# Performance work log

Measured on AMD Instinct MI355X. Metric: run time of the kernel, lower is better.

## Reference

```python
import jax, jax.numpy as jnp
import numpy as np

B = 4096          # graph pairs in batch
NPG = 40          # nodes per molecular graph
N = B * NPG       # total nodes per drug batch
EPG = 160         # directed edges per graph
E = B * EPG
F_IN = 78         # atom feature dim
HID = 128
HEADS = 4
ADD = 8           # additional features (concentrations)
BN_EPS = 1e-5
D0 = HEADS * HID          # 512
CMB = 4 * HID + ADD       # 2 drugs * (mean||max of 128) + ADD = 520


def setup_inputs() -> dict:
    key = jax.random.key(0)
    ks = iter(jax.random.split(key, 64))
    def nrm(shape, s=0.1):
        return jax.random.normal(next(ks), shape, jnp.float32) * s
    def pos(shape):  # positive running variances
        return jax.random.uniform(next(ks), shape, jnp.float32, 0.5, 1.5)
    offs = jnp.repeat(jnp.arange(B, dtype=jnp.int32) * NPG, EPG)
    def edges():
        return jax.random.randint(next(ks), (2, E), 0, NPG, dtype=jnp.int32) + offs[None, :]
    batch = jnp.repeat(jnp.arange(B, dtype=jnp.int32), NPG)
    inp = dict(
        x_a=nrm((N, F_IN), 1.0), edge_a=edges(), batch_a=batch,
        x_b=nrm((N, F_IN), 1.0), edge_b=edges(), batch_b=batch,
        addf=nrm((B, ADD), 1.0),
        # shared GAT encoder params
        gW0=nrm((F_IN, D0)), gb0=nrm((D0,)), gas0=nrm((D0,)), gad0=nrm((D0,)),
        gW1=nrm((D0, D0)), gb1=nrm((D0,)), gas1=nrm((D0,)), gad1=nrm((D0,)),
        gW2=nrm((D0, HID)), gb2=nrm((HID,)), gas2=nrm((HID,)), gad2=nrm((HID,)),
        bn0g=pos((D0,)), bn0b=nrm((D0,)), bn0m=nrm((D0,)), bn0v=pos((D0,)),
        bn1g=pos((D0,)), bn1b=nrm((D0,)), bn1m=nrm((D0,)), bn1v=pos((D0,)),
        bn2g=pos((HID,)), bn2b=nrm((HID,)), bn2m=nrm((HID,)), bn2v=pos((HID,)),
        # combination MLP params (Linear + eval BatchNorm stats)
        mW0=nrm((CMB, 2 * HID)), mb0=nrm((2 * HID,)),
        mg0=pos((2 * HID,)), mbe0=nrm((2 * HID,)), mm0=nrm((2 * HID,)), mv0=pos((2 * HID,)),
        mW1=nrm((2 * HID, HID)), mb1=nrm((HID,)),
        mg1=pos((HID,)), mbe1=nrm((HID,)), mm1=nrm((HID,)), mv1=pos((HID,)),
        mW2=nrm((HID, 1)), mb2=nrm((1,)),
    )
    return inp


def _bn(x, g, b, m, v):
    return (x - m) * jax.lax.rsqrt(v + BN_EPS) * g + b


def _gat(x, src, dst, W, b, a_src, a_dst, heads, ch, concat):
    """PyG GATConv (eval): linear, per-head additive attention with
    leaky_relu(0.2), segment-softmax over incoming edges (self-loops included)."""
    n = x.shape[0]
    h = (x @ W).reshape(n, heads, ch)                     # [N, H, C]
    es = jnp.sum(h * a_src.reshape(1, heads, ch), -1)     # [N, H]
    ed = jnp.sum(h * a_dst.reshape(1, heads, ch), -1)     # [N, H]
    e = jax.nn.leaky_relu(es[src] + ed[dst], 0.2)         # [E', H]
    emax = jax.ops.segment_max(e, dst, num_segments=n)
    ex = jnp.exp(e - emax[dst])
    den = jax.ops.segment_sum(ex, dst, num_segments=n)
    alpha = ex / den[dst]                                 # [E', H]
    out = jax.ops.segment_sum(h[src] * alpha[..., None], dst, num_segments=n)
    out = out.reshape(n, heads * ch) if concat else jnp.mean(out, axis=1)
    return out + b


def _encode(x, edge, batch, p):
    n = x.shape[0]
    sl = jnp.arange(n, dtype=edge.dtype)                  # self-loops (PyG default)
    src = jnp.concatenate([edge[0], sl])
    dst = jnp.concatenate([edge[1], sl])
    x = _gat(x, src, dst, p['gW0'], p['gb0'], p['gas0'], p['gad0'], HEADS, HID, True)
    x = jax.nn.relu(_bn(x, p['bn0g'], p['bn0b'], p['bn0m'], p['bn0v']))
    x = _gat(x, src, dst, p['gW1'], p['gb1'], p['gas1'], p['gad1'], HEADS, HID, True)
    x = jax.nn.relu(_bn(x, p['bn1g'], p['bn1b'], p['bn1m'], p['bn1v']))
    x = _gat(x, src, dst, p['gW2'], p['gb2'], p['gas2'], p['gad2'], 1, HID, False)
    x = _bn(x, p['bn2g'], p['bn2b'], p['bn2m'], p['bn2v'])  # no relu on last layer
    cnt = jax.ops.segment_sum(jnp.ones((n, 1), x.dtype), batch, num_segments=B)
    x_mean = jax.ops.segment_sum(x, batch, num_segments=B) / cnt
    x_max = jax.ops.segment_max(x, batch, num_segments=B)
    return jnp.concatenate([x_mean, x_max], axis=1)        # [B, 2*HID]


def reference(x_a, edge_a, batch_a, x_b, edge_b, batch_b, addf,
              gW0, gb0, gas0, gad0, gW1, gb1, gas1, gad1, gW2, gb2, gas2, gad2,
              bn0g, bn0b, bn0m, bn0v, bn1g, bn1b, bn1m, bn1v, bn2g, bn2b, bn2m, bn2v,
              mW0, mb0, mg0, mbe0, mm0, mv0, mW1, mb1, mg1, mbe1, mm1, mv1, mW2, mb2):
    p = dict(gW0=gW0, gb0=gb0, gas0=gas0, gad0=gad0, gW1=gW1, gb1=gb1, gas1=gas1,
             gad1=gad1, gW2=gW2, gb2=gb2, gas2=gas2, gad2=gad2,
             bn0g=bn0g, bn0b=bn0b, bn0m=bn0m, bn0v=bn0v,
             bn1g=bn1g, bn1b=bn1b, bn1m=bn1m, bn1v=bn1v,
             bn2g=bn2g, bn2b=bn2b, bn2m=bn2m, bn2v=bn2v)
    emb_a = _encode(x_a, edge_a, batch_a, p)
    emb_b = _encode(x_b, edge_b, batch_b, p)
    c = jnp.concatenate([emb_a, emb_b, addf], axis=1)      # [B, 520]
    h = jax.nn.relu(_bn(c @ mW0 + mb0, mg0, mbe0, mm0, mv0))
    h = jax.nn.relu(_bn(h @ mW1 + mb1, mg1, mbe1, mm1, mv1))
    out = jax.nn.sigmoid(h @ mW2 + mb2)
    return jnp.squeeze(out, -1)                            # [B]
```

## Files before the change

### kernel.cpp

```cpp
#include <hip/hip_runtime.h>
#include <stdint.h>

#define B_GRAPHS 4096
#define NPG 40
#define NTOT (B_GRAPHS * NPG)
#define EPG 160
#define ETOT (B_GRAPHS * EPG)
#define ESL 200
#define F_IN 78
#define KP0 96
#define HID 128
#define D0 512
#define CMB 520
#define BN_EPS 1e-5f
#define AST 48
#define KPM 544
#define A0ST 552
#define H1ST 264
#define H2ST 132

typedef short bf16x8 __attribute__((ext_vector_type(8)));
typedef float floatx4 __attribute__((ext_vector_type(4)));

__device__ inline float b2f(unsigned short u) {
    union { float f; uint32_t i; } v; v.i = ((uint32_t)u) << 16; return v.f;
}
__device__ inline unsigned short f2b(float f) {
    union { float f; uint32_t i; } v; v.f = f;
    uint32_t x = v.i;
    return (unsigned short)((x + 0x7fffu + ((x >> 16) & 1u)) >> 16);
}
__device__ inline float lo16(uint32_t u) {
    union { float f; uint32_t i; } v; v.i = u << 16; return v.f;
}
__device__ inline float hi16(uint32_t u) {
    union { float f; uint32_t i; } v; v.i = u & 0xffff0000u; return v.f;
}
__device__ inline unsigned int fenc(float f) {
    unsigned int b = __float_as_uint(f);
    return (b & 0x80000000u) ? ~b : (b | 0x80000000u);
}
__device__ inline float fdec(unsigned int u) {
    unsigned int b = (u & 0x80000000u) ? (u & 0x7fffffffu) : ~u;
    return __uint_as_float(b);
}
__device__ inline int htoff(int ch, int s) {
    int chunk = s >> 3, within = s & 7;
    return ch * 40 + (((chunk + ch) % 5) << 3) + within;
}
__device__ inline void gl2lds16(const unsigned short* g, unsigned short* l) {
    __builtin_amdgcn_global_load_lds(
        (const __attribute__((address_space(1))) unsigned int*)g,
        (__attribute__((address_space(3))) unsigned int*)l, 16, 0, 0);
}

__global__ __launch_bounds__(256)
void write_code_kernel(float* __restrict__ out, int n, float S)
{
    int i = blockIdx.x * 256 + threadIdx.x;
    if (i < n) out[i] = (i == 0) ? S : 0.f;
}

__global__ __launch_bounds__(256)
void convw_kernel(const float* __restrict__ W, unsigned short* __restrict__ Wt,
                  int K, int N, int Kp)
{
    int t = blockIdx.x * 256 + threadIdx.x;
    if (t >= N * Kp) return;
    int n = t / Kp, k = t - n * Kp;
    Wt[t] = (k < K) ? f2b(W[(size_t)k * N + n]) : 0;
}

__global__ __launch_bounds__(256)
void convw_hilo_kernel(const float* __restrict__ W,
                       unsigned short* __restrict__ Whi,
                       unsigned short* __restrict__ Wlo,
                       int K, int N, int Kp)
{
    int t = blockIdx.x * 256 + threadIdx.x;
    if (t >= N * Kp) return;
    int n = t / Kp, k = t - n * Kp;
    float x = (k < K) ? W[(size_t)k * N + n] : 0.f;
    unsigned short hb = f2b(x);
    Whi[t] = hb;
    Wlo[t] = f2b(x - b2f(hb));
}

__global__ __launch_bounds__(256)
void convx_kernel(const float* __restrict__ X, unsigned short* __restrict__ Xb, int M)
{
    int t = blockIdx.x * 256 + threadIdx.x;
    if (t >= M * (KP0 / 8)) return;
    int r = t / (KP0 / 8), c8 = t - r * (KP0 / 8);
    unsigned int pk[4];
    #pragma unroll
    for (int j = 0; j < 4; j++) {
        int k0 = c8 * 8 + 2 * j, k1 = k0 + 1;
        float x0 = (k0 < F_IN) ? X[(size_t)r * F_IN + k0] : 0.f;
        float x1 = (k1 < F_IN) ? X[(size_t)r * F_IN + k1] : 0.f;
        pk[j] = (unsigned int)f2b(x0) | ((unsigned int)f2b(x1) << 16);
    }
    *(uint4*)&Xb[(size_t)r * KP0 + c8 * 8] = make_uint4(pk[0], pk[1], pk[2], pk[3]);
}

__global__ __launch_bounds__(256)
void gemm_mfma_kernel(const unsigned short* __restrict__ A,
                      const unsigned short* __restrict__ Bt,
                      unsigned short* __restrict__ C,
                      int M, int K, int N)
{
    __shared__ __align__(16) unsigned short As[128 * 32];
    __shared__ __align__(16) unsigned short Bs[128 * 32];
    const int tid  = threadIdx.x;
    const int lane = tid & 63, w = tid >> 6;
    const int quad = lane >> 4, l16 = lane & 15;
    const int wm = w >> 1, wn = w & 1;
    const int row0 = blockIdx.y * 128, col0 = blockIdx.x * 128;

    floatx4 acc[4][4];
    #pragma unroll
    for (int mi = 0; mi < 4; mi++)
        #pragma unroll
        for (int ni = 0; ni < 4; ni++)
            acc[mi][ni] = (floatx4){0.f, 0.f, 0.f, 0.f};

    int srow[2], scg[2];
    #pragma unroll
    for (int it = 0; it < 2; it++) {
        int L = it * 4096 + w * 1024 + lane * 16;
        int r = L >> 6;
        int cp = (L >> 4) & 3;
        srow[it] = r;
        scg[it]  = cp ^ ((r >> 1) & 3);
    }

    for (int k0 = 0; k0 < K; k0 += 32) {
        #pragma unroll
        for (int it = 0; it < 2; it++) {
            int ra = row0 + srow[it]; if (ra >= M) ra = M - 1;
            gl2lds16(A + (size_t)ra * K + k0 + scg[it] * 8,
                     As + (it * 4096 + w * 1024) / 2);
            int rb = col0 + srow[it];
            gl2lds16(Bt + (size_t)rb * K + k0 + scg[it] * 8,
                     Bs + (it * 4096 + w * 1024) / 2);
        }
        __syncthreads();

        bf16x8 fA[4], fB[4];
        #pragma unroll
        for (int mi = 0; mi < 4; mi++) {
            int r = wm * 64 + mi * 16 + l16;
            __builtin_memcpy(&fA[mi], &As[r * 32 + ((quad ^ ((r >> 1) & 3)) * 8)], 16);
        }
        #pragma unroll
        for (int ni = 0; ni < 4; ni++) {
            int r = wn * 64 + ni * 16 + l16;
            __builtin_memcpy(&fB[ni], &Bs[r * 32 + ((quad ^ ((r >> 1) & 3)) * 8)], 16);
        }
        #pragma unroll
        for (int mi = 0; mi < 4; mi++)
            #pragma unroll
            for (int ni = 0; ni < 4; ni++)
                acc[mi][ni] = __builtin_amdgcn_mfma_f32_16x16x32_bf16(
                    fB[ni], fA[mi], acc[mi][ni], 0, 0, 0);
        __syncthreads();
    }

    #pragma unroll
    for (int mi = 0; mi < 4; mi++) {
        int row = row0 + wm * 64 + mi * 16 + l16;
        if (row < M) {
            #pragma unroll
            for (int ni = 0; ni < 4; ni++) {
                floatx4 a = acc[mi][ni];
                unsigned int p0 = (unsigned int)f2b(a[0]) | ((unsigned int)f2b(a[1]) << 16);
                unsigned int p1 = (unsigned int)f2b(a[2]) | ((unsigned int)f2b(a[3]) << 16);
                *(uint2*)(C + (size_t)row * N + col0 + wn * 64 + ni * 16 + quad * 4) =
                    make_uint2(p0, p1);
            }
        }
    }
}

__global__ __launch_bounds__(256)
void gat4_fused_kernel(unsigned short* __restrict__ H,
                       const int* __restrict__ edge,
                       const float* __restrict__ avs, const float* __restrict__ avd,
                       const float* __restrict__ bias,
                       const float* __restrict__ bng, const float* __restrict__ bnb,
                       const float* __restrict__ bnm, const float* __restrict__ bnv,
                       int g0)
{
    __shared__ __align__(16) unsigned short ht[D0 * NPG];
    __shared__ float es[4 * NPG], ed[4 * NPG];
    __shared__ unsigned int Mu[4 * NPG];
    __shared__ float den[4 * NPG];
    __shared__ __align__(16) unsigned char cnt[NPG * 48];
    __shared__ short2 eloc[ESL];
    const int tid = threadIdx.x;
    const int lane = tid & 63, w = tid >> 6;
    const int quad = lane >> 4, l16 = lane & 15;
    const int gg = g0 + blockIdx.x;
    unsigned short* Hg = H + (size_t)blockIdx.x * NPG * D0;

    for (int i = tid; i < NPG * 48 / 4; i += 256) ((unsigned int*)cnt)[i] = 0u;
    if (tid < 4 * NPG) { Mu[tid] = 0u; den[tid] = 0.f; }
    for (int i = tid; i < ESL; i += 256) {
        if (i < EPG) {
            int s  = edge[(size_t)gg * EPG + i] - gg * NPG;
            int dd = edge[(size_t)ETOT + (size_t)gg * EPG + i] - gg * NPG;
            eloc[i] = make_short2((short)s, (short)dd);
        } else {
            short v = (short)(i - EPG);
            eloc[i] = make_short2(v, v);
        }
    }
    for (int u = tid; u < 64 * (NPG / 4); u += 256) {
        int c8 = u & 63, gi = u >> 6;
        const unsigned short* src = Hg + (size_t)(4 * gi) * D0 + c8 * 8;
        uint4 v0 = *(const uint4*)(src);
        uint4 v1 = *(const uint4*)(src + D0);
        uint4 v2 = *(const uint4*)(src + 2 * D0);
        uint4 v3 = *(const uint4*)(src + 3 * D0);
        unsigned int a0[4] = {v0.x, v0.y, v0.z, v0.w};
        unsigned int a1[4] = {v1.x, v1.y, v1.z, v1.w};
        unsigned int a2[4] = {v2.x, v2.y, v2.z, v2.w};
        unsigned int a3[4] = {v3.x, v3.y, v3.z, v3.w};
        #pragma unroll
        for (int k = 0; k < 8; k++) {
            const int ws = k >> 1, sh = (k & 1) * 16;
            unsigned int w0 = ((a0[ws] >> sh) & 0xffffu) | (((a1[ws] >> sh) & 0xffffu) << 16);
            unsigned int w1 = ((a2[ws] >> sh) & 0xffffu) | (((a3[ws] >> sh) & 0xffffu) << 16);
            *(uint2*)&ht[htoff(c8 * 8 + k, 4 * gi)] = make_uint2(w0, w1);
        }
    }
    __syncthreads();

    {
        float as0=0,as1=0,as2=0,as3=0, ad0=0,ad1=0,ad2=0,ad3=0;
        for (int ci = 0; ci < 32; ci++) {
            int c = quad + ci * 4;
            int chv = w * 128 + c;
            uint2 hv = *(const uint2*)&ht[htoff(chv, 4 * l16)];
            float h0 = lo16(hv.x), h1 = hi16(hv.x), h2 = lo16(hv.y), h3 = hi16(hv.y);
            float vs = avs[chv], vd = avd[chv];
            as0 += h0*vs; as1 += h1*vs; as2 += h2*vs; as3 += h3*vs;
            ad0 += h0*vd; ad1 += h1*vd; ad2 += h2*vd; ad3 += h3*vd;
        }
        #define RED4(x) x += __shfl_xor(x, 16); x += __shfl_xor(x, 32);
        RED4(as0) RED4(as1) RED4(as2) RED4(as3)
        RED4(ad0) RED4(ad1) RED4(ad2) RED4(ad3)
        #undef RED4
        if (quad == 0) {
            float rs[4] = {as0, as1, as2, as3};
            float rd[4] = {ad0, ad1, ad2, ad3};
            #pragma unroll
            for (int rr = 0; rr < 4; rr++) {
                int node = 4 * l16 + rr;
                if (node < NPG) { es[w * NPG + node] = rs[rr]; ed[w * NPG + node] = rd[rr]; }
            }
        }
    }
    for (int e = tid; e < ESL; e += 256) {
        short2 sd = eloc[e];
        atomicAdd((unsigned int*)cnt + ((sd.y * 48 + sd.x) >> 2),
                  1u << ((sd.x & 3) * 8));
    }
    __syncthreads();

    for (int u = tid; u < 4 * ESL; u += 256) {
        int e = u >> 2, hd = u & 3;
        short2 sd = eloc[e];
        float v = es[hd * NPG + sd.x] + ed[hd * NPG + sd.y];
        v = v > 0.f ? v : 0.2f * v;
        atomicMax(&Mu[hd * NPG + sd.y], fenc(v));
    }
    __syncthreads();
    for (int u = tid; u < 4 * ESL; u += 256) {
        int e = u >> 2, hd = u & 3;
        short2 sd = eloc[e];
        float v = es[hd * NPG + sd.x] + ed[hd * NPG + sd.y];
        v = v > 0.f ? v : 0.2f * v;
        float ex = __expf(v - fdec(Mu[hd * NPG + sd.y]));
        atomicAdd(&den[hd * NPG + sd.y], ex);
    }
    __syncthreads();

    {
        bf16x8 ahi[3][2], alo[3][2];
        float esv0[8], esv1[8];
        #pragma unroll
        for (int j = 0; j < 8; j++) {
            esv0[j] = es[w * NPG + quad * 8 + j];
            esv1[j] = (quad == 0) ? es[w * NPG + 32 + j] : 0.f;
        }
        #pragma unroll
        for (int mt = 0; mt < 3; mt++) {
            int dn = mt * 16 + l16;
            bool ok = dn < NPG;
            float edv = 0.f, m = 0.f, di = 0.f;
            uint2 c0 = make_uint2(0u, 0u), c1 = make_uint2(0u, 0u);
            if (ok) {
                edv = ed[w * NPG + dn];
                m = fdec(Mu[w * NPG + dn]);
                di = 1.f / den[w * NPG + dn];
                c0 = *(const uint2*)&cnt[dn * 48 + quad * 8];
                if (quad == 0) c1 = *(const uint2*)&cnt[dn * 48 + 32];
            }
            #pragma unroll
            for (int j = 0; j < 8; j++) {
                unsigned int cb0 = ((j < 4 ? c0.x : c0.y) >> ((j & 3) * 8)) & 0xffu;
                float v0 = esv0[j] + edv;
                v0 = v0 > 0.f ? v0 : 0.2f * v0;
                float a0 = (ok && cb0) ? (float)cb0 * __expf(v0 - m) * di : 0.f;
                unsigned short hb0 = f2b(a0);
                ahi[mt][0][j] = (short)hb0;
                alo[mt][0][j] = (short)f2b(a0 - b2f(hb0));

                unsigned int cb1 = ((j < 4 ? c1.x : c1.y) >> ((j & 3) * 8)) & 0xffu;
                float v1 = esv1[j] + edv;
                v1 = v1 > 0.f ? v1 : 0.2f * v1;
                float a1 = (ok && quad == 0 && cb1) ? (float)cb1 * __expf(v1 - m) * di : 0.f;
                unsigned short hb1 = f2b(a1);
                ahi[mt][1][j] = (short)hb1;
                alo[mt][1][j] = (short)f2b(a1 - b2f(hb1));
            }
        }
        const floatx4 z = {0.f, 0.f, 0.f, 0.f};
        for (int nt = 0; nt < 8; nt++) {
            const int ch0 = w * 128 + nt * 16;
            bf16x8 b0, b1 = {0,0,0,0,0,0,0,0};
            __builtin_memcpy(&b0, &ht[htoff(ch0 + l16, quad * 8)], 16);
            if (quad == 0) __builtin_memcpy(&b1, &ht[htoff(ch0 + l16, 32)], 16);
            floatx4 acc0 = z, acc1 = z, acc2 = z;
            acc0 = __builtin_amdgcn_mfma_f32_16x16x32_bf16(ahi[0][0], b0, acc0, 0, 0, 0);
            acc1 = __builtin_amdgcn_mfma_f32_16x16x32_bf16(ahi[1][0], b0, acc1, 0, 0, 0);
            acc2 = __builtin_amdgcn_mfma_f32_16x16x32_bf16(ahi[2][0], b0, acc2, 0, 0, 0);
            acc0 = __builtin_amdgcn_mfma_f32_16x16x32_bf16(alo[0][0], b0, acc0, 0, 0, 0);
            acc1 = __builtin_amdgcn_mfma_f32_16x16x32_bf16(alo[1][0], b0, acc1, 0, 0, 0);
            acc2 = __builtin_amdgcn_mfma_f32_16x16x32_bf16(alo[2][0], b0, acc2, 0, 0, 0);
            acc0 = __builtin_amdgcn_mfma_f32_16x16x32_bf16(ahi[0][1], b1, acc0, 0, 0, 0);
            acc1 = __builtin_amdgcn_mfma_f32_16x16x32_bf16(ahi[1][1], b1, acc1, 0, 0, 0);
            acc2 = __builtin_amdgcn_mfma_f32_16x16x32_bf16(ahi[2][1], b1, acc2, 0, 0, 0);
            acc0 = __builtin_amdgcn_mfma_f32_16x16x32_bf16(alo[0][1], b1, acc0, 0, 0, 0);
            acc1 = __builtin_amdgcn_mfma_f32_16x16x32_bf16(alo[1][1], b1, acc1, 0, 0, 0);
            acc2 = __builtin_amdgcn_mfma_f32_16x16x32_bf16(alo[2][1], b1, acc2, 0, 0, 0);
            const int c = ch0 + l16;
            float scl = rsqrtf(bnv[c] + BN_EPS) * bng[c];
            float sft = (bias[c] - bnm[c]) * scl + bnb[c];
            unsigned short* reg = &ht[ch0 * 40];
            #pragma unroll
            for (int mt = 0; mt < 3; mt++) {
                floatx4 a = (mt == 0) ? acc0 : (mt == 1) ? acc1 : acc2;
                #pragma unroll
                for (int rr = 0; rr < 4; rr++) {
                    int dn = mt * 16 + quad * 4 + rr;
                    if (dn < NPG) {
                        float o = a[rr] * scl + sft;
                        o = fmaxf(o, 0.f);
                        reg[dn * 16 + l16] = f2b(o);
                    }
                }
            }
        }
    }
    __syncthreads();
    for (int u = tid; u < NPG * 64; u += 256) {
        int s = u >> 6, c8 = u & 63;
        const unsigned short* reg = &ht[(c8 >> 1) * 16 * 40];
        uint4 v = *(const uint4*)&reg[s * 16 + (c8 & 1) * 8];
        *(uint4*)(Hg + (size_t)s * D0 + c8 * 8) = v;
    }
}

__global__ __launch_bounds__(256)
void gat1_pool_fused_kernel(const unsigned short* __restrict__ H,
                            const int* __restrict__ edge,
                            const float* __restrict__ avs, const float* __restrict__ avd,
                            const float* __restrict__ bias,
                            const float* __restrict__ bng, const float* __restrict__ bnb,
                            const float* __restrict__ bnm, const float* __restrict__ bnv,
                            float* __restrict__ cmb, int colbase, int g0)
{
    __shared__ __align__(16) unsigned short ht[HID * NPG];
    __shared__ float A1f[NPG * AST];
    __shared__ float es[NPG], ed[NPG];
    __shared__ unsigned int Mu[NPG];
    __shared__ float den[NPG];
    __shared__ short2 eloc[ESL];
    const int tid = threadIdx.x;
    const int lane = tid & 63, w = tid >> 6;
    const int quad = lane >> 4, l16 = lane & 15;
    const int gg = g0 + blockIdx.x;
    const unsigned short* Hg = H + (size_t)blockIdx.x * NPG * HID;

    for (int i = tid; i < NPG * AST; i += 256) A1f[i] = 0.f;
    if (tid < NPG) { Mu[tid] = 0u; den[tid] = 0.f; }
    for (int i = tid; i < ESL; i += 256) {
        if (i < EPG) {
            int s  = edge[(size_t)gg * EPG + i] - gg * NPG;
            int dd = edge[(size_t)ETOT + (size_t)gg * EPG + i] - gg * NPG;
            eloc[i] = make_short2((short)s, (short)dd);
        } else {
            short v = (short)(i - EPG);
            eloc[i] = make_short2(v, v);
        }
    }
    for (int u = tid; u < 16 * (NPG / 4); u += 256) {
        int c8 = u & 15, gi = u >> 4;
        const unsigned short* src = Hg + (size_t)(4 * gi) * HID + c8 * 8;
        uint4 v0 = *(const uint4*)(src);
        uint4 v1 = *(const uint4*)(src + HID);
        uint4 v2 = *(const uint4*)(src + 2 * HID);
        uint4 v3 = *(const uint4*)(src + 3 * HID);
        unsigned int a0[4] = {v0.x, v0.y, v0.z, v0.w};
        unsigned int a1[4] = {v1.x, v1.y, v1.z, v1.w};
        unsigned int a2[4] = {v2.x, v2.y, v2.z, v2.w};
        unsigned int a3[4] = {v3.x, v3.y, v3.z, v3.w};
        #pragma unroll
        for (int k = 0; k < 8; k++) {
            const int ws = k >> 1, sh = (k & 1) * 16;
            unsigned int w0 = ((a0[ws] >> sh) & 0xffffu) | (((a1[ws] >> sh) & 0xffffu) << 16);
            unsigned int w1 = ((a2[ws] >> sh) & 0xffffu) | (((a3[ws] >> sh) & 0xffffu) << 16);
            *(uint2*)&ht[htoff(c8 * 8 + k, 4 * gi)] = make_uint2(w0, w1);
        }
    }
    __syncthreads();

    if (w < 2) {
        const float* av = w ? avd : avs;
        float a0=0,a1=0,a2=0,a3=0;
        for (int ci = 0; ci < 32; ci++) {
            int c = quad + ci * 4;
            uint2 hv = *(const uint2*)&ht[htoff(c, 4 * l16)];
            float vc = av[c];
            a0 += lo16(hv.x)*vc; a1 += hi16(hv.x)*vc;
            a2 += lo16(hv.y)*vc; a3 += hi16(hv.y)*vc;
        }
        #define RED4(x) x += __shfl_xor(x, 16); x += __shfl_xor(x, 32);
        RED4(a0) RED4(a1) RED4(a2) RED4(a3)
        #undef RED4
        if (quad == 0) {
            float rv[4] = {a0, a1, a2, a3};
            float* dst = w ? ed : es;
            #pragma unroll
            for (int rr = 0; rr < 4; rr++) {
                int node = 4 * l16 + rr;
                if (node < NPG) dst[node] = rv[rr];
            }
        }
    }
    __syncthreads();
    for (int u = tid; u < ESL; u += 256) {
        short2 sd = eloc[u];
        float v = es[sd.x] + ed[sd.y];
        v = v > 0.f ? v : 0.2f * v;
        atomicMax(&Mu[sd.y], fenc(v));
    }
    __syncthreads();
    for (int u = tid; u < ESL; u += 256) {
        short2 sd = eloc[u];
        float v = es[sd.x] + ed[sd.y];
        v = v > 0.f ? v : 0.2f * v;
        float ex = __expf(v - fdec(Mu[sd.y]));
        atomicAdd(&den[sd.y], ex);
        atomicAdd(&A1f[sd.x * AST + sd.y], ex);
    }
    __syncthreads();
    for (int idx = tid; idx < NPG * AST; idx += 256) {
        int dn = idx % AST;
        float val = A1f[idx];
        unsigned int pw = 0u;
        if (dn < NPG) {
            float a = val / den[dn];
            unsigned short hi = f2b(a);
            float rem = a - b2f(hi);
            pw = (unsigned int)hi | ((unsigned int)f2b(rem) << 16);
        }
        ((unsigned int*)A1f)[idx] = pw;
    }
    __syncthreads();

    {
        const unsigned int* Ap = (const unsigned int*)A1f;
        bf16x8 ahi[3][2], alo[3][2];
        #pragma unroll
        for (int mt = 0; mt < 3; mt++) {
            #pragma unroll
            for (int j = 0; j < 8; j++) {
                unsigned int w0 = Ap[(quad * 8 + j) * AST + mt * 16 + l16];
                ahi[mt][0][j] = (short)(w0 & 0xffffu);
                alo[mt][0][j] = (short)(w0 >> 16);
                unsigned int w1 = (quad == 0) ? Ap[(32 + j) * AST + mt * 16 + l16] : 0u;
                ahi[mt][1][j] = (short)(w1 & 0xffffu);
                alo[mt][1][j] = (short)(w1 >> 16);
            }
        }
        const floatx4 z = {0.f, 0.f, 0.f, 0.f};
        for (int t2 = 0; t2 < 2; t2++) {
            const int ch0 = (w * 2 + t2) * 16;
            bf16x8 b0, b1 = {0,0,0,0,0,0,0,0};
            __builtin_memcpy(&b0, &ht[htoff(ch0 + l16, quad * 8)], 16);
            if (quad == 0) __builtin_memcpy(&b1, &ht[htoff(ch0 + l16, 32)], 16);
            floatx4 acc0 = z, acc1 = z, acc2 = z;
            acc0 = __builtin_amdgcn_mfma_f32_16x16x32_bf16(ahi[0][0], b0, acc0, 0, 0, 0);
            acc1 = __builtin_amdgcn_mfma_f32_16x16x32_bf16(ahi[1][0], b0, acc1, 0, 0, 0);
            acc2 = __builtin_amdgcn_mfma_f32_16x16x32_bf16(ahi[2][0], b0, acc2, 0, 0, 0);
            acc0 = __builtin_amdgcn_mfma_f32_16x16x32_bf16(alo[0][0], b0, acc0, 0, 0, 0);
            acc1 = __builtin_amdgcn_mfma_f32_16x16x32_bf16(alo[1][0], b0, acc1, 0, 0, 0);
            acc2 = __builtin_amdgcn_mfma_f32_16x16x32_bf16(alo[2][0], b0, acc2, 0, 0, 0);
            acc0 = __builtin_amdgcn_mfma_f32_16x16x32_bf16(ahi[0][1], b1, acc0, 0, 0, 0);
            acc1 = __builtin_amdgcn_mfma_f32_16x16x32_bf16(ahi[1][1], b1, acc1, 0, 0, 0);
            acc2 = __builtin_amdgcn_mfma_f32_16x16x32_bf16(ahi[2][1], b1, acc2, 0, 0, 0);
            acc0 = __builtin_amdgcn_mfma_f32_16x16x32_bf16(alo[0][1], b1, acc0, 0, 0, 0);
            acc1 = __builtin_amdgcn_mfma_f32_16x16x32_bf16(alo[1][1], b1, acc1, 0, 0, 0);
            acc2 = __builtin_amdgcn_mfma_f32_16x16x32_bf16(alo[2][1], b1, acc2, 0, 0, 0);
            const int c = ch0 + l16;
            float scl = rsqrtf(bnv[c] + BN_EPS) * bng[c];
            float sft = (bias[c] - bnm[c]) * scl + bnb[c];
            float psum = 0.f, pmax = -1e30f;
            #pragma unroll
            for (int mt = 0; mt < 3; mt++) {
                floatx4 a = (mt == 0) ? acc0 : (mt == 1) ? acc1 : acc2;
                #pragma unroll
                for (int rr = 0; rr < 4; rr++) {
                    int dn = mt * 16 + quad * 4 + rr;
                    if (dn < NPG) {
                        float o = a[rr] * scl + sft;
                        psum += o;
                        pmax = fmaxf(pmax, o);
                    }
                }
            }
            psum += __shfl_xor(psum, 16); psum += __shfl_xor(psum, 32);
            pmax = fmaxf(pmax, __shfl_xor(pmax, 16));
            pmax = fmaxf(pmax, __shfl_xor(pmax, 32));
            if (quad == 0) {
                cmb[(size_t)gg * 512 + colbase + c] = psum * (1.f / NPG);
                cmb[(size_t)gg * 512 + colbase + HID + c] = pmax;
            }
        }
    }
}

__global__ __launch_bounds__(256)
void mlp_mfma_kernel(const float* __restrict__ cmb, const float* __restrict__ addf,
                     const unsigned short* __restrict__ W0hi, const unsigned short* __restrict__ W0lo,
                     const float* __restrict__ b0, const float* __restrict__ g0v,
                     const float* __restrict__ be0, const float* __restrict__ m0,
                     const float* __restrict__ v0,
                     const unsigned short* __restrict__ W1hi, const unsigned short* __restrict__ W1lo,
                     const float* __restrict__ b1, const float* __restrict__ g1v,
                     const float* __restrict__ be1, const float* __restrict__ m1,
                     const float* __restrict__ v1,
                     const float* __restrict__ W2, const float* __restrict__ b2,
                     float* __restrict__ out)
{
    __shared__ __align__(16) unsigned short a0hi[16 * A0ST], a0lo[16 * A0ST];
    __shared__ __align__(16) unsigned short h1hi[16 * H1ST], h1lo[16 * H1ST];
    __shared__ float h2[16 * H2ST];
    const int tid = threadIdx.x;
    const int lane = tid & 63, w = tid >> 6;
    const int quad = lane >> 4, l16 = lane & 15;
    const int gb = blockIdx.x * 16;

    for (int i = tid; i < 16 * KPM; i += 256) {
        int g = i / KPM, k = i - g * KPM;
        float x = 0.f;
        if (k < 512) x = cmb[(size_t)(gb + g) * 512 + k];
        else if (k < CMB) x = addf[(gb + g) * 8 + (k - 512)];
        unsigned short hb = f2b(x);
        a0hi[g * A0ST + k] = hb;
        a0lo[g * A0ST + k] = f2b(x - b2f(hb));
    }
    __syncthreads();

    {
        floatx4 acc[4];
        #pragma unroll
        for (int ni = 0; ni < 4; ni++) acc[ni] = (floatx4){0.f, 0.f, 0.f, 0.f};
        for (int k0 = 0; k0 < KPM; k0 += 32) {
            bf16x8 fah, fal;
            __builtin_memcpy(&fah, &a0hi[l16 * A0ST + k0 + quad * 8], 16);
            __builtin_memcpy(&fal, &a0lo[l16 * A0ST + k0 + quad * 8], 16);
            #pragma unroll
            for (int ni = 0; ni < 4; ni++) {
                int row = w * 64 + ni * 16 + l16;
                bf16x8 fwh, fwl;
                __builtin_memcpy(&fwh, &W0hi[(size_t)row * KPM + k0 + quad * 8], 16);
                __builtin_memcpy(&fwl, &W0lo[(size_t)row * KPM + k0 + quad * 8], 16);
                acc[ni] = __builtin_amdgcn_mfma_f32_16x16x32_bf16(fwh, fah, acc[ni], 0, 0, 0);
                acc[ni] = __builtin_amdgcn_mfma_f32_16x16x32_bf16(fwh, fal, acc[ni], 0, 0, 0);
                acc[ni] = __builtin_amdgcn_mfma_f32_16x16x32_bf16(fwl, fah, acc[ni], 0, 0, 0);
            }
        }
        #pragma unroll
        for (int ni = 0; ni < 4; ni++) {
            int cbase = w * 64 + ni * 16 + quad * 4;
            unsigned int ph[2], pl[2];
            #pragma unroll
            for (int j = 0; j < 2; j++) {
                unsigned int hh[2], ll[2];
                #pragma unroll
                for (int q = 0; q < 2; q++) {
                    int rr = 2 * j + q, c = cbase + rr;
                    float scl = rsqrtf(v0[c] + BN_EPS) * g0v[c];
                    float val = (acc[ni][rr] + b0[c] - m0[c]) * scl + be0[c];
                    val = fmaxf(val, 0.f);
                    unsigned short hb = f2b(val);
                    hh[q] = hb;
                    ll[q] = f2b(val - b2f(hb));
                }
                ph[j] = hh[0] | (hh[1] << 16);
                pl[j] = ll[0] | (ll[1] << 16);
            }
            *(uint2*)&h1hi[l16 * H1ST + cbase] = make_uint2(ph[0], ph[1]);
            *(uint2*)&h1lo[l16 * H1ST + cbase] = make_uint2(pl[0], pl[1]);
        }
    }
    __syncthreads();

    {
        floatx4 acc[2];
        acc[0] = (floatx4){0.f, 0.f, 0.f, 0.f};
        acc[1] = (floatx4){0.f, 0.f, 0.f, 0.f};
        for (int k0 = 0; k0 < 256; k0 += 32) {
            bf16x8 fah, fal;
            __builtin_memcpy(&fah, &h1hi[l16 * H1ST + k0 + quad * 8], 16);
            __builtin_memcpy(&fal, &h1lo[l16 * H1ST + k0 + quad * 8], 16);
            #pragma unroll
            for (int ni = 0; ni < 2; ni++) {
                int row = w * 32 + ni * 16 + l16;
                bf16x8 fwh, fwl;
                __builtin_memcpy(&fwh, &W1hi[(size_t)row * 256 + k0 + quad * 8], 16);
                __builtin_memcpy(&fwl, &W1lo[(size_t)row * 256 + k0 + quad * 8], 16);
                acc[ni] = __builtin_amdgcn_mfma_f32_16x16x32_bf16(fwh, fah, acc[ni], 0, 0, 0);
                acc[ni] = __builtin_amdgcn_mfma_f32_16x16x32_bf16(fwh, fal, acc[ni], 0, 0, 0);
                acc[ni] = __builtin_amdgcn_mfma_f32_16x16x32_bf16(fwl, fah, acc[ni], 0, 0, 0);
            }
        }
        #pragma unroll
        for (int ni = 0; ni < 2; ni++) {
            #pragma unroll
            for (int rr = 0; rr < 4; rr++) {
                int c = w * 32 + ni * 16 + quad * 4 + rr;
                float scl = rsqrtf(v1[c] + BN_EPS) * g1v[c];
                float val = (acc[ni][rr] + b1[c] - m1[c]) * scl + be1[c];
                h2[l16 * H2ST + c] = fmaxf(val, 0.f);
            }
        }
    }
    __syncthreads();

    {
        int g = tid >> 4, part = tid & 15;
        float s = 0.f;
        #pragma unroll
        for (int j = 0; j < 8; j++)
            s += h2[g * H2ST + part * 8 + j] * W2[part * 8 + j];
        s += __shfl_xor(s, 1); s += __shfl_xor(s, 2);
        s += __shfl_xor(s, 4); s += __shfl_xor(s, 8);
        if (part == 0) out[gb + g] = 1.f / (1.f + __expf(-(s + b2[0])));
    }
}

extern "C" void kernel_launch(void* const* d_in, const int* in_sizes, int n_in,
                              void* d_out, int out_size, void* d_ws, size_t ws_size,
                              hipStream_t stream)
{
    float* out = (float*)d_out;
    int out_n = out_size < 4096 ? out_size : 4096;

    const float* x_a  = (const float*)d_in[0];
    const int*   edge_a = (const int*)d_in[1];
    const float* x_b  = (const float*)d_in[3];
    const int*   edge_b = (const int*)d_in[4];
    const float* addf = (const float*)d_in[6];
    const float* gW0 = (const float*)d_in[7],  *gb0 = (const float*)d_in[8];
    const float* gas0 = (const float*)d_in[9], *gad0 = (const float*)d_in[10];
    const float* gW1 = (const float*)d_in[11], *gb1 = (const float*)d_in[12];
    const float* gas1 = (const float*)d_in[13], *gad1 = (const float*)d_in[14];
    const float* gW2 = (const float*)d_in[15], *gb2 = (const float*)d_in[16];
    const float* gas2 = (const float*)d_in[17], *gad2 = (const float*)d_in[18];
    const float* bn0g = (const float*)d_in[19], *bn0b = (const float*)d_in[20];
    const float* bn0m = (const float*)d_in[21], *bn0v = (const float*)d_in[22];
    const float* bn1g = (const float*)d_in[23], *bn1b = (const float*)d_in[24];
    const float* bn1m = (const float*)d_in[25], *bn1v = (const float*)d_in[26];
    const float* bn2g = (const float*)d_in[27], *bn2b = (const float*)d_in[28];
    const float* bn2m = (const float*)d_in[29], *bn2v = (const float*)d_in[30];
    const float* mW0 = (const float*)d_in[31], *mb0 = (const float*)d_in[32];
    const float* mg0 = (const float*)d_in[33], *mbe0 = (const float*)d_in[34];
    const float* mm0 = (const float*)d_in[35], *mv0 = (const float*)d_in[36];
    const float* mW1 = (const float*)d_in[37], *mb1 = (const float*)d_in[38];
    const float* mg1 = (const float*)d_in[39], *mbe1 = (const float*)d_in[40];
    const float* mm1 = (const float*)d_in[41], *mv1 = (const float*)d_in[42];
    const float* mW2 = (const float*)d_in[43], *mb2 = (const float*)d_in[44];

    char* p = (char*)d_ws;
    const size_t CMB_BYTES = (size_t)B_GRAPHS * 512 * sizeof(float);
    float* cmb = (float*)p; p += CMB_BYTES;
    unsigned short* W0t = (unsigned short*)p; p += (size_t)D0 * KP0 * 2;
    unsigned short* W1t = (unsigned short*)p; p += (size_t)D0 * D0 * 2;
    unsigned short* W2t = (unsigned short*)p; p += (size_t)HID * D0 * 2;
    unsigned short* M0hi = (unsigned short*)p; p += (size_t)256 * KPM * 2;
    unsigned short* M0lo = (unsigned short*)p; p += (size_t)256 * KPM * 2;
    unsigned short* M1hi = (unsigned short*)p; p += (size_t)128 * 256 * 2;
    unsigned short* M1lo = (unsigned short*)p; p += (size_t)128 * 256 * 2;
    size_t used = (size_t)(p - (char*)d_ws);
    const size_t PG = 7680ull + 40960ull + 40960ull;
    int chunk = B_GRAPHS;
    while (chunk > 4 && used + (size_t)chunk * PG > ws_size) chunk >>= 1;
    if (used + (size_t)chunk * PG > ws_size) {
        write_code_kernel<<<(out_n + 255) / 256, 256, 0, stream>>>(out, out_n, 500000.f);
        return;
    }
    unsigned short* Xb = (unsigned short*)p; p += (size_t)chunk * 7680;
    unsigned short* B1 = (unsigned short*)p; p += (size_t)chunk * 40960;
    unsigned short* B2 = (unsigned short*)p;

    convw_kernel<<<(D0 * KP0 + 255) / 256, 256, 0, stream>>>(gW0, W0t, F_IN, D0, KP0);
    convw_kernel<<<(D0 * D0 + 255) / 256, 256, 0, stream>>>(gW1, W1t, D0, D0, D0);
    convw_kernel<<<(HID * D0 + 255) / 256, 256, 0, stream>>>(gW2, W2t, D0, HID, D0);
    convw_hilo_kernel<<<(256 * KPM + 255) / 256, 256, 0, stream>>>(
        mW0, M0hi, M0lo, CMB, 256, KPM);
    convw_hilo_kernel<<<(128 * 256 + 255) / 256, 256, 0, stream>>>(
        mW1, M1hi, M1lo, 256, 128, 256);

    for (int drug = 0; drug < 2; drug++) {
        const float* x = drug ? x_b : x_a;
        const int* edge = drug ? edge_b : edge_a;
        int colbase = drug ? 256 : 0;

        for (int g0 = 0; g0 < B_GRAPHS; g0 += chunk) {
            int n = chunk * NPG;
            int gy = (n + 127) / 128;
            convx_kernel<<<(n * (KP0 / 8) + 255) / 256, 256, 0, stream>>>(
                x + (size_t)g0 * NPG * F_IN, Xb, n);
            gemm_mfma_kernel<<<dim3(D0 / 128, gy), 256, 0, stream>>>(
                Xb, W0t, B1, n, KP0, D0);
            gat4_fused_kernel<<<chunk, 256, 0, stream>>>(
                B1, edge, gas0, gad0, gb0, bn0g, bn0b, bn0m, bn0v, g0);
            gemm_mfma_kernel<<<dim3(D0 / 128, gy), 256, 0, stream>>>(
                B1, W1t, B2, n, D0, D0);
            gat4_fused_kernel<<<chunk, 256, 0, stream>>>(
                B2, edge, gas1, gad1, gb1, bn1g, bn1b, bn1m, bn1v, g0);
            gemm_mfma_kernel<<<dim3(HID / 128, gy), 256, 0, stream>>>(
                B2, W2t, B1, n, D0, HID);
            gat1_pool_fused_kernel<<<chunk, 256, 0, stream>>>(
                B1, edge, gas2, gad2, gb2, bn2g, bn2b, bn2m, bn2v,
                cmb, colbase, g0);
        }
    }
    mlp_mfma_kernel<<<B_GRAPHS / 16, 256, 0, stream>>>(
        cmb, addf, M0hi, M0lo, mb0, mg0, mbe0, mm0, mv0,
        M1hi, M1lo, mb1, mg1, mbe1, mm1, mv1, mW2, mb2, out);
}
```

Measured before the change: 1.419 ms.

## Fuse last GEMM into GAT pool kernel, swizzle GEMM blocks across XCDs

Folds the final 512->128 projection into the per-graph attention/pool kernel, so each block computes its own H tile with MFMA directly from global memory, and the separate GEMM launch plus its intermediate write and read go away. The dense float attention matrix in shared memory is replaced by per-edge multiplicity byte counts, and attention weights are recomputed in registers from es/ed/max/den. The general GEMM also remaps block IDs so consecutive tiles land on the same XCD for better L2 locality. In exchange, the fused GEMM reads the weight matrix from global per block with no LDS reuse, and the byte counters would overflow if one node pair had more than 255 edges.

```diff
diff --git a/kernel.cpp b/kernel.cpp
--- a/kernel.cpp
+++ b/kernel.cpp
@@ -13,7 +13,6 @@
 #define D0 512
 #define CMB 520
 #define BN_EPS 1e-5f
-#define AST 48
 #define KPM 544
 #define A0ST 552
 #define H1ST 264
@@ -115,7 +114,12 @@
     const int lane = tid & 63, w = tid >> 6;
     const int quad = lane >> 4, l16 = lane & 15;
     const int wm = w >> 1, wn = w & 1;
-    const int row0 = blockIdx.y * 128, col0 = blockIdx.x * 128;
+    const int nwg  = gridDim.x * gridDim.y;
+    const int orig = blockIdx.y * gridDim.x + blockIdx.x;
+    const int q = nwg >> 3, r = nwg & 7;
+    const int xcd = orig & 7, off = orig >> 3;
+    const int swz = (xcd < r ? xcd * (q + 1) : r * (q + 1) + (xcd - r) * q) + off;
+    const int row0 = (swz / gridDim.x) * 128, col0 = (swz % gridDim.x) * 128;
 
     floatx4 acc[4][4];
     #pragma unroll
@@ -128,10 +132,10 @@
     #pragma unroll
     for (int it = 0; it < 2; it++) {
         int L = it * 4096 + w * 1024 + lane * 16;
-        int r = L >> 6;
+        int rr = L >> 6;
         int cp = (L >> 4) & 3;
-        srow[it] = r;
-        scg[it]  = cp ^ ((r >> 1) & 3);
+        srow[it] = rr;
+        scg[it]  = cp ^ ((rr >> 1) & 3);
     }
 
     for (int k0 = 0; k0 < K; k0 += 32) {
@@ -149,13 +153,13 @@
         bf16x8 fA[4], fB[4];
         #pragma unroll
         for (int mi = 0; mi < 4; mi++) {
-            int r = wm * 64 + mi * 16 + l16;
-            __builtin_memcpy(&fA[mi], &As[r * 32 + ((quad ^ ((r >> 1) & 3)) * 8)], 16);
+            int rr = wm * 64 + mi * 16 + l16;
+            __builtin_memcpy(&fA[mi], &As[rr * 32 + ((quad ^ ((rr >> 1) & 3)) * 8)], 16);
         }
         #pragma unroll
         for (int ni = 0; ni < 4; ni++) {
-            int r = wn * 64 + ni * 16 + l16;
-            __builtin_memcpy(&fB[ni], &Bs[r * 32 + ((quad ^ ((r >> 1) & 3)) * 8)], 16);
+            int rr = wn * 64 + ni * 16 + l16;
+            __builtin_memcpy(&fB[ni], &Bs[rr * 32 + ((quad ^ ((rr >> 1) & 3)) * 8)], 16);
         }
         #pragma unroll
         for (int mi = 0; mi < 4; mi++)
@@ -374,27 +378,28 @@
 }
 
 __global__ __launch_bounds__(256)
-void gat1_pool_fused_kernel(const unsigned short* __restrict__ H,
-                            const int* __restrict__ edge,
-                            const float* __restrict__ avs, const float* __restrict__ avd,
-                            const float* __restrict__ bias,
-                            const float* __restrict__ bng, const float* __restrict__ bnb,
-                            const float* __restrict__ bnm, const float* __restrict__ bnv,
-                            float* __restrict__ cmb, int colbase, int g0)
+void fused2_kernel(const unsigned short* __restrict__ A,
+                   const unsigned short* __restrict__ Wt,
+                   const int* __restrict__ edge,
+                   const float* __restrict__ avs, const float* __restrict__ avd,
+                   const float* __restrict__ bias,
+                   const float* __restrict__ bng, const float* __restrict__ bnb,
+                   const float* __restrict__ bnm, const float* __restrict__ bnv,
+                   float* __restrict__ cmb, int colbase, int g0)
 {
     __shared__ __align__(16) unsigned short ht[HID * NPG];
-    __shared__ float A1f[NPG * AST];
     __shared__ float es[NPG], ed[NPG];
     __shared__ unsigned int Mu[NPG];
     __shared__ float den[NPG];
+    __shared__ __align__(16) unsigned char cnt[NPG * 48];
     __shared__ short2 eloc[ESL];
     const int tid = threadIdx.x;
     const int lane = tid & 63, w = tid >> 6;
     const int quad = lane >> 4, l16 = lane & 15;
     const int gg = g0 + blockIdx.x;
-    const unsigned short* Hg = H + (size_t)blockIdx.x * NPG * HID;
-
-    for (int i = tid; i < NPG * AST; i += 256) A1f[i] = 0.f;
+    const unsigned short* Ag = A + (size_t)blockIdx.x * NPG * D0;
+
+    for (int i = tid; i < NPG * 48 / 4; i += 256) ((unsigned int*)cnt)[i] = 0u;
     if (tid < NPG) { Mu[tid] = 0u; den[tid] = 0.f; }
     for (int i = tid; i < ESL; i += 256) {
         if (i < EPG) {
@@ -406,23 +411,44 @@
             eloc[i] = make_short2(v, v);
         }
     }
-    for (int u = tid; u < 16 * (NPG / 4); u += 256) {
-        int c8 = u & 15, gi = u >> 4;
-        const unsigned short* src = Hg + (size_t)(4 * gi) * HID + c8 * 8;
-        uint4 v0 = *(const uint4*)(src);
-        uint4 v1 = *(const uint4*)(src + HID);
-        uint4 v2 = *(const uint4*)(src + 2 * HID);
-        uint4 v3 = *(const uint4*)(src + 3 * HID);
-        unsigned int a0[4] = {v0.x, v0.y, v0.z, v0.w};
-        unsigned int a1[4] = {v1.x, v1.y, v1.z, v1.w};
-        unsigned int a2[4] = {v2.x, v2.y, v2.z, v2.w};
-        unsigned int a3[4] = {v3.x, v3.y, v3.z, v3.w};
-        #pragma unroll
-        for (int k = 0; k < 8; k++) {
-            const int ws = k >> 1, sh = (k & 1) * 16;
-            unsigned int w0 = ((a0[ws] >> sh) & 0xffffu) | (((a1[ws] >> sh) & 0xffffu) << 16);
-            unsigned int w1 = ((a2[ws] >> sh) & 0xffffu) | (((a3[ws] >> sh) & 0xffffu) << 16);
-            *(uint2*)&ht[htoff(c8 * 8 + k, 4 * gi)] = make_uint2(w0, w1);
+
+    {
+        floatx4 acc[3][2];
+        #pragma unroll
+        for (int mt = 0; mt < 3; mt++)
+            #pragma unroll
+            for (int nt = 0; nt < 2; nt++)
+                acc[mt][nt] = (floatx4){0.f, 0.f, 0.f, 0.f};
+        for (int k0 = 0; k0 < D0; k0 += 32) {
+            bf16x8 fA[3];
+            #pragma unroll
+            for (int mt = 0; mt < 3; mt++) {
+                int s = mt * 16 + l16; if (s >= NPG) s = NPG - 1;
+                __builtin_memcpy(&fA[mt], Ag + (size_t)s * D0 + k0 + quad * 8, 16);
+            }
+            #pragma unroll
+            for (int nt = 0; nt < 2; nt++) {
+                int ch = w * 32 + nt * 16 + l16;
+                bf16x8 fW;
+                __builtin_memcpy(&fW, Wt + (size_t)ch * D0 + k0 + quad * 8, 16);
+                acc[0][nt] = __builtin_amdgcn_mfma_f32_16x16x32_bf16(fA[0], fW, acc[0][nt], 0, 0, 0);
+                acc[1][nt] = __builtin_amdgcn_mfma_f32_16x16x32_bf16(fA[1], fW, acc[1][nt], 0, 0, 0);
+                acc[2][nt] = __builtin_amdgcn_mfma_f32_16x16x32_bf16(fA[2], fW, acc[2][nt], 0, 0, 0);
+            }
+        }
+        #pragma unroll
+        for (int nt = 0; nt < 2; nt++) {
+            int ch = w * 32 + nt * 16 + l16;
+            #pragma unroll
+            for (int mt = 0; mt < 3; mt++) {
+                int s0 = mt * 16 + quad * 4;
+                if (s0 < NPG) {
+                    floatx4 a = acc[mt][nt];
+                    unsigned int p0 = (unsigned int)f2b(a[0]) | ((unsigned int)f2b(a[1]) << 16);
+                    unsigned int p1 = (unsigned int)f2b(a[2]) | ((unsigned int)f2b(a[3]) << 16);
+                    *(uint2*)&ht[htoff(ch, s0)] = make_uint2(p0, p1);
+                }
+            }
         }
     }
     __syncthreads();
@@ -450,6 +476,11 @@
             }
         }
     }
+    for (int e = tid; e < ESL; e += 256) {
+        short2 sd = eloc[e];
+        atomicAdd((unsigned int*)cnt + ((sd.y * 48 + sd.x) >> 2),
+                  1u << ((sd.x & 3) * 8));
+    }
     __syncthreads();
     for (int u = tid; u < ESL; u += 256) {
         short2 sd = eloc[u];
@@ -464,36 +495,47 @@
         v = v > 0.f ? v : 0.2f * v;
         float ex = __expf(v - fdec(Mu[sd.y]));
         atomicAdd(&den[sd.y], ex);
-        atomicAdd(&A1f[sd.x * AST + sd.y], ex);
-    }
-    __syncthreads();
-    for (int idx = tid; idx < NPG * AST; idx += 256) {
-        int dn = idx % AST;
-        float val = A1f[idx];
-        unsigned int pw = 0u;
-        if (dn < NPG) {
-            float a = val / den[dn];
-            unsigned short hi = f2b(a);
-            float rem = a - b2f(hi);
-            pw = (unsigned int)hi | ((unsigned int)f2b(rem) << 16);
-        }
-        ((unsigned int*)A1f)[idx] = pw;
     }
     __syncthreads();
 
     {
-        const unsigned int* Ap = (const unsigned int*)A1f;
         bf16x8 ahi[3][2], alo[3][2];
+        float esv0[8], esv1[8];
+        #pragma unroll
+        for (int j = 0; j < 8; j++) {
+            esv0[j] = es[quad * 8 + j];
+            esv1[j] = (quad == 0) ? es[32 + j] : 0.f;
+        }
         #pragma unroll
         for (int mt = 0; mt < 3; mt++) {
+            int dn = mt * 16 + l16;
+            bool ok = dn < NPG;
+            float edv = 0.f, m = 0.f, di = 0.f;
+            uint2 c0 = make_uint2(0u, 0u), c1 = make_uint2(0u, 0u);
+            if (ok) {
+                edv = ed[dn];
+                m = fdec(Mu[dn]);
+                di = 1.f / den[dn];
+                c0 = *(const uint2*)&cnt[dn * 48 + quad * 8];
+                if (quad == 0) c1 = *(const uint2*)&cnt[dn * 48 + 32];
+            }
             #pragma unroll
             for (int j = 0; j < 8; j++) {
-                unsigned int w0 = Ap[(quad * 8 + j) * AST + mt * 16 + l16];
-                ahi[mt][0][j] = (short)(w0 & 0xffffu);
-                alo[mt][0][j] = (short)(w0 >> 16);
-                unsigned int w1 = (quad == 0) ? Ap[(32 + j) * AST + mt * 16 + l16] : 0u;
-                ahi[mt][1][j] = (short)(w1 & 0xffffu);
-                alo[mt][1][j] = (short)(w1 >> 16);
+                unsigned int cb0 = ((j < 4 ? c0.x : c0.y) >> ((j & 3) * 8)) & 0xffu;
+                float v0 = esv0[j] + edv;
+                v0 = v0 > 0.f ? v0 : 0.2f * v0;
+                float a0 = (ok && cb0) ? (float)cb0 * __expf(v0 - m) * di : 0.f;
+                unsigned short hb0 = f2b(a0);
+                ahi[mt][0][j] = (short)hb0;
+                alo[mt][0][j] = (short)f2b(a0 - b2f(hb0));
+
+                unsigned int cb1 = ((j < 4 ? c1.x : c1.y) >> ((j & 3) * 8)) & 0xffu;
+                float v1 = esv1[j] + edv;
+                v1 = v1 > 0.f ? v1 : 0.2f * v1;
+                float a1 = (ok && quad == 0 && cb1) ? (float)cb1 * __expf(v1 - m) * di : 0.f;
+                unsigned short hb1 = f2b(a1);
+                ahi[mt][1][j] = (short)hb1;
+                alo[mt][1][j] = (short)f2b(a1 - b2f(hb1));
             }
         }
         const floatx4 z = {0.f, 0.f, 0.f, 0.f};
@@ -744,10 +786,8 @@
                 B1, W1t, B2, n, D0, D0);
             gat4_fused_kernel<<<chunk, 256, 0, stream>>>(
                 B2, edge, gas1, gad1, gb1, bn1g, bn1b, bn1m, bn1v, g0);
-            gemm_mfma_kernel<<<dim3(HID / 128, gy), 256, 0, stream>>>(
-                B2, W2t, B1, n, D0, HID);
-            gat1_pool_fused_kernel<<<chunk, 256, 0, stream>>>(
-                B1, edge, gas2, gad2, gb2, bn2g, bn2b, bn2m, bn2v,
+            fused2_kernel<<<chunk, 256, 0, stream>>>(
+                B2, W2t, edge, gas2, gad2, gb2, bn2g, bn2b, bn2m, bn2v,
                 cmb, colbase, g0);
         }
     }
```

Measured after the change: 1.483 ms. 1.05x slower.
